# Performance work log

Measured on AMD Instinct MI355X. Metric: run time of the kernel, lower is better.

Reference implementation:

```python
import jax, jax.numpy as jnp
import numpy as np

C = 512          # in_channels == key_channels
K_REGIONS = 256  # number of proxy/object regions
N, H, Wd = 8, 128, 128


def _cba(x, w, sc, bi):
    """1x1 Conv + (folded) BN + ReLU. x: [n, Cin, h, w], w: [Cout, Cin]."""
    y = jnp.einsum('nchw,oc->nohw', x, w)
    return jax.nn.relu(sc[None, :, None, None] * y + bi[None, :, None, None])


def setup_inputs() -> dict:
    key = jax.random.key(0)
    kx, kp, kw, ks, kb = jax.random.split(key, 5)
    x = jax.random.normal(kx, (N, C, H, Wd), dtype=jnp.float32)
    proxy = jax.random.normal(kp, (N, C, K_REGIONS, 1), dtype=jnp.float32)
    # 7 ConvBnAct layers: [fp0, fp1, fo0, fo1, fd0, fd1, fup]
    W = jax.random.normal(kw, (7, C, C), dtype=jnp.float32) * (1.0 / np.sqrt(C))
    s = jax.random.uniform(ks, (7, C), dtype=jnp.float32, minval=0.5, maxval=1.5)
    b = jax.random.normal(kb, (7, C), dtype=jnp.float32) * 0.02
    return {'x': x, 'proxy': proxy, 'W': W, 's': s, 'b': b}


def reference(x, proxy, W, s, b):
    n, _, h, w = x.shape
    # f_pixel(x): two 1x1 ConvBnAct -> query [n, HW, C]
    q = _cba(_cba(x, W[0], s[0], b[0]), W[1], s[1], b[1])
    query = q.reshape(n, C, h * w).transpose(0, 2, 1)          # [n, HW, C]
    # f_object(proxy) -> key [n, C, K]
    k = _cba(_cba(proxy, W[2], s[2], b[2]), W[3], s[3], b[3])
    key_t = k.reshape(n, C, -1)                                 # [n, C, K]
    # f_down(proxy) -> value [n, K, C]
    v = _cba(_cba(proxy, W[4], s[4], b[4]), W[5], s[5], b[5])
    value = v.reshape(n, C, -1).transpose(0, 2, 1)              # [n, K, C]
    # scaled dot-product attention (single head, unmasked)
    sim = jnp.einsum('nqc,nck->nqk', query, key_t) * (C ** -0.5)
    sim = jax.nn.softmax(sim, axis=-1)                          # [n, HW, K]
    context = jnp.einsum('nqk,nkc->nqc', sim, value)            # [n, HW, C]
    context = context.transpose(0, 2, 1).reshape(n, C, h, w)
    # f_up
    return _cba(context, W[6], s[6], b[6])
```

## Files before the change

### kernel.cpp

```cpp
#include <hip/hip_runtime.h>
#include <hip/hip_bf16.h>
#include <stdint.h>

typedef __bf16 bf16;
typedef __bf16 bf16x8 __attribute__((ext_vector_type(8)));
typedef __bf16 bf16x4v __attribute__((ext_vector_type(4)));
typedef float f32x4 __attribute__((ext_vector_type(4)));

#define AS1 __attribute__((address_space(1)))
#define AS3 __attribute__((address_space(3)))

__device__ __forceinline__ void g2lds16(const bf16* g, bf16* l) {
  __builtin_amdgcn_global_load_lds((AS1 void*)(uintptr_t)g, (AS3 void*)l, 16, 0, 0);
}

__global__ void prep_weights_k(const float* __restrict__ W, const float* __restrict__ s,
                               const float* __restrict__ b, bf16* __restrict__ Wb,
                               float* __restrict__ bb) {
  int idx = blockIdx.x * 256 + threadIdx.x;
  int c = idx & 511;
  int o = (idx >> 9) & 511;
  int l = idx >> 18;
  const float r = 0.04419417382415922f;
  float f = (l == 3) ? r : 1.0f;
  Wb[idx] = (bf16)(W[idx] * s[(l << 9) + o] * f);
  if (c == 0) bb[(l << 9) + o] = b[(l << 9) + o] * f;
}

__global__ void transpose_cast_k(const float* __restrict__ in, bf16* __restrict__ out,
                                 int R, int Cc) {
  __shared__ float tile[32][33];
  int c0 = blockIdx.x * 32, r0 = blockIdx.y * 32;
  size_t zoff = (size_t)blockIdx.z * R * Cc;
  int tx = threadIdx.x, ty = threadIdx.y;
#pragma unroll
  for (int i = 0; i < 32; i += 8)
    tile[ty + i][tx] = in[zoff + (size_t)(r0 + ty + i) * Cc + c0 + tx];
  __syncthreads();
#pragma unroll
  for (int i = 0; i < 32; i += 8)
    out[zoff + (size_t)(c0 + ty + i) * R + r0 + tx] = (bf16)tile[tx][ty + i];
}

__global__ void softmax_k(const float* __restrict__ sim, bf16* __restrict__ P) {
  int row = blockIdx.x * 4 + (threadIdx.x >> 6);
  int lane = threadIdx.x & 63;
  const float4 v = ((const float4*)(sim + (size_t)row * 256))[lane];
  float m = fmaxf(fmaxf(v.x, v.y), fmaxf(v.z, v.w));
#pragma unroll
  for (int o = 32; o > 0; o >>= 1) m = fmaxf(m, __shfl_xor(m, o));
  float e0 = __expf(v.x - m), e1 = __expf(v.y - m);
  float e2 = __expf(v.z - m), e3 = __expf(v.w - m);
  float sum = e0 + e1 + e2 + e3;
#pragma unroll
  for (int o = 32; o > 0; o >>= 1) sum += __shfl_xor(sum, o);
  float inv = 1.0f / sum;
  bf16x4v pk;
  pk.x = (bf16)(e0 * inv); pk.y = (bf16)(e1 * inv);
  pk.z = (bf16)(e2 * inv); pk.w = (bf16)(e3 * inv);
  ((bf16x4v*)(P + (size_t)row * 256))[lane] = pk;
}

template <bool RELU, bool OUTF32, int BIASMODE>
__global__ __launch_bounds__(256, 2) void gemm_nt(
    const bf16* __restrict__ A, long sAb,
    const bf16* __restrict__ B, long sBb,
    void* __restrict__ OUT, long sOb,
    const float* __restrict__ bias,
    int M, int N, int Kd) {
  __shared__ bf16 sA[128][64];
  __shared__ bf16 sB[128][64];
  const int n0 = blockIdx.x * 128;
  const int m0 = blockIdx.y * 128;
  const bf16* Ab = A + (size_t)blockIdx.z * sAb;
  const bf16* Bb = B + (size_t)blockIdx.z * sBb;
  const int t = threadIdx.x;
  const int lane = t & 63;
  const int w = t >> 6;
  const int wm = (w & 1) << 6;
  const int wn = (w >> 1) << 6;
  const int srow = t >> 3;
  const int scol = (t & 7) << 3;

  f32x4 acc[4][4] = {};

  const int fr = lane & 15;
  const int fq = (lane >> 4) << 3;

  for (int k0 = 0; k0 < Kd; k0 += 64) {
#pragma unroll
    for (int i = 0; i < 4; i++) {
      g2lds16(Ab + (size_t)(m0 + i * 32 + srow) * Kd + (k0 + scol), &sA[i * 32 + srow][scol]);
      g2lds16(Bb + (size_t)(n0 + i * 32 + srow) * Kd + (k0 + scol), &sB[i * 32 + srow][scol]);
    }
    __syncthreads();
#pragma unroll
    for (int kk = 0; kk < 64; kk += 32) {
      bf16x8 af[4], bfv[4];
#pragma unroll
      for (int i = 0; i < 4; i++) af[i] = *(const bf16x8*)&sA[wm + i * 16 + fr][kk + fq];
#pragma unroll
      for (int j = 0; j < 4; j++) bfv[j] = *(const bf16x8*)&sB[wn + j * 16 + fr][kk + fq];
#pragma unroll
      for (int i = 0; i < 4; i++)
#pragma unroll
        for (int j = 0; j < 4; j++)
          acc[i][j] = __builtin_amdgcn_mfma_f32_16x16x32_bf16(af[i], bfv[j], acc[i][j], 0, 0, 0);
    }
    __syncthreads();
  }

  const int rb = m0 + wm + ((lane >> 4) << 2);
  const int cb = n0 + wn + (lane & 15);
#pragma unroll
  for (int i = 0; i < 4; i++) {
#pragma unroll
    for (int r = 0; r < 4; r++) {
      const int orow = rb + i * 16 + r;
#pragma unroll
      for (int j = 0; j < 4; j++) {
        const int oc = cb + j * 16;
        float vv = acc[i][j][r];
        if (BIASMODE == 1) vv += bias[oc];
        else if (BIASMODE == 2) vv += bias[orow];
        if (RELU) vv = fmaxf(vv, 0.0f);
        if (OUTF32)
          ((float*)OUT)[(size_t)blockIdx.z * sOb + (size_t)orow * N + oc] = vv;
        else
          ((bf16*)OUT)[(size_t)blockIdx.z * sOb + (size_t)orow * N + oc] = (bf16)vv;
      }
    }
  }
}

extern "C" void kernel_launch(void* const* d_in, const int* in_sizes, int n_in,
                              void* d_out, int out_size, void* d_ws, size_t ws_size,
                              hipStream_t stream) {
  const float* x = (const float*)d_in[0];
  const float* proxy = (const float*)d_in[1];
  const float* W = (const float*)d_in[2];
  const float* s = (const float*)d_in[3];
  const float* b = (const float*)d_in[4];
  float* out = (float*)d_out;

  const int C = 512, K = 256, NB = 8, HW = 16384;
  const size_t MiB = 1024 * 1024;
  char* ws = (char*)d_ws;
  if (ws_size < 272 * MiB) return;

  bf16* Wb   = (bf16*)(ws + 0);
  float* bb  = (float*)(ws + 3670016);
  bf16* pT   = (bf16*)(ws + 4 * MiB);
  bf16* k1   = (bf16*)(ws + 6 * MiB);
  bf16* key  = (bf16*)(ws + 8 * MiB);
  bf16* t2   = (bf16*)(ws + 10 * MiB);
  bf16* v    = (bf16*)(ws + 12 * MiB);
  bf16* bufA = (bf16*)(ws + 16 * MiB);
  bf16* bufB = (bf16*)(ws + 144 * MiB);

  bf16* xb  = bufA;
  bf16* t0  = bufB;
  bf16* q   = bufA;
  float* simf = (float*)bufB;
  bf16* P   = bufA;
  bf16* ctx = bufB;

  const long KC = (long)K * C;
  const long HWC = (long)HW * C;
  const long HWK = (long)HW * K;

  prep_weights_k<<<7 * 512 * 512 / 256, 256, 0, stream>>>(W, s, b, Wb, bb);
  transpose_cast_k<<<dim3(K / 32, C / 32, NB), dim3(32, 8), 0, stream>>>(proxy, pT, C, K);
  transpose_cast_k<<<dim3(HW / 32, C / 32, NB), dim3(32, 8), 0, stream>>>(x, xb, C, HW);
  gemm_nt<true, false, 1><<<dim3(C / 128, K / 128, NB), 256, 0, stream>>>(
      pT, KC, Wb + 2 * 262144, 0, k1, KC, bb + 2 * 512, K, C, C);
  gemm_nt<true, false, 1><<<dim3(C / 128, K / 128, NB), 256, 0, stream>>>(
      k1, KC, Wb + 3 * 262144, 0, key, KC, bb + 3 * 512, K, C, C);
  gemm_nt<true, false, 1><<<dim3(C / 128, K / 128, NB), 256, 0, stream>>>(
      pT, KC, Wb + 4 * 262144, 0, t2, KC, bb + 4 * 512, K, C, C);
  gemm_nt<true, false, 2><<<dim3(K / 128, C / 128, NB), 256, 0, stream>>>(
      Wb + 5 * 262144, 0, t2, KC, v, (long)C * K, bb + 5 * 512, C, K, C);
  gemm_nt<true, false, 1><<<dim3(C / 128, HW / 128, NB), 256, 0, stream>>>(
      xb, HWC, Wb, 0, t0, HWC, bb, HW, C, C);
  gemm_nt<true, false, 1><<<dim3(C / 128, HW / 128, NB), 256, 0, stream>>>(
      t0, HWC, Wb + 1 * 262144, 0, q, HWC, bb + 512, HW, C, C);
  gemm_nt<false, true, 0><<<dim3(K / 128, HW / 128, NB), 256, 0, stream>>>(
      q, HWC, key, KC, simf, HWK, nullptr, HW, K, C);
  softmax_k<<<NB * HW / 4, 256, 0, stream>>>(simf, P);
  gemm_nt<false, false, 0><<<dim3(C / 128, HW / 128, NB), 256, 0, stream>>>(
      P, HWK, v, (long)C * K, ctx, HWC, nullptr, HW, C, K);
  gemm_nt<true, true, 2><<<dim3(HW / 128, C / 128, NB), 256, 0, stream>>>(
      Wb + 6 * 262144, 0, ctx, HWC, out, HWC, bb + 6 * 512, C, HW, C);
}
```

Baseline: 1.017 ms.

## Fuse QK^T, softmax and PV into one attention kernel; merge proxy GEMMs

Replaces the separate sim GEMM (fp32 output), softmax kernel and PV GEMM with a single kernel. It computes a 64-row score tile in registers, applies softmax there and multiplies by V from LDS, so the large fp32 similarity matrix and the bf16 probability matrix never go through HBM. It also concatenates the fo0 and fd0 weights so both proxy first-layer convs run as one GEMM with strided leading dimensions. The transpose kernel is widened to 64x64 tiles with float4 loads. The risk is that the fused kernel rereads the full key and V per 64-row block with little overlap, and uses 64KB of LDS, which limits occupancy.

```diff
diff --git a/kernel.cpp b/kernel.cpp
--- a/kernel.cpp
+++ b/kernel.cpp
@@ -16,55 +16,54 @@
 
 __global__ void prep_weights_k(const float* __restrict__ W, const float* __restrict__ s,
                                const float* __restrict__ b, bf16* __restrict__ Wb,
-                               float* __restrict__ bb) {
+                               float* __restrict__ bb, bf16* __restrict__ W24,
+                               float* __restrict__ b24) {
   int idx = blockIdx.x * 256 + threadIdx.x;
   int c = idx & 511;
   int o = (idx >> 9) & 511;
   int l = idx >> 18;
   const float r = 0.04419417382415922f;
   float f = (l == 3) ? r : 1.0f;
-  Wb[idx] = (bf16)(W[idx] * s[(l << 9) + o] * f);
-  if (c == 0) bb[(l << 9) + o] = b[(l << 9) + o] * f;
+  float wv = W[idx] * s[(l << 9) + o] * f;
+  float bv = b[(l << 9) + o] * f;
+  Wb[idx] = (bf16)wv;
+  if (c == 0) bb[(l << 9) + o] = bv;
+  if (l == 2) { W24[(size_t)o * 512 + c] = (bf16)wv;         if (c == 0) b24[o] = bv; }
+  if (l == 4) { W24[(size_t)(512 + o) * 512 + c] = (bf16)wv; if (c == 0) b24[512 + o] = bv; }
 }
 
 __global__ void transpose_cast_k(const float* __restrict__ in, bf16* __restrict__ out,
-                                 int R, int Cc) {
-  __shared__ float tile[32][33];
-  int c0 = blockIdx.x * 32, r0 = blockIdx.y * 32;
-  size_t zoff = (size_t)blockIdx.z * R * Cc;
-  int tx = threadIdx.x, ty = threadIdx.y;
-#pragma unroll
-  for (int i = 0; i < 32; i += 8)
-    tile[ty + i][tx] = in[zoff + (size_t)(r0 + ty + i) * Cc + c0 + tx];
+                                 int R, int S) {
+  __shared__ float tile[64][65];
+  int s0 = blockIdx.x * 64, r0 = blockIdx.y * 64;
+  size_t zo = (size_t)blockIdx.z * R * S;
+  int t = threadIdx.x;
+  int rr = t >> 4, cc = t & 15;
+#pragma unroll
+  for (int i = 0; i < 4; i++) {
+    float4 v = *(const float4*)&in[zo + (size_t)(r0 + rr + 16 * i) * S + s0 + cc * 4];
+    tile[rr + 16 * i][cc * 4 + 0] = v.x;
+    tile[rr + 16 * i][cc * 4 + 1] = v.y;
+    tile[rr + 16 * i][cc * 4 + 2] = v.z;
+    tile[rr + 16 * i][cc * 4 + 3] = v.w;
+  }
   __syncthreads();
 #pragma unroll
-  for (int i = 0; i < 32; i += 8)
-    out[zoff + (size_t)(c0 + ty + i) * R + r0 + tx] = (bf16)tile[tx][ty + i];
-}
-
-__global__ void softmax_k(const float* __restrict__ sim, bf16* __restrict__ P) {
-  int row = blockIdx.x * 4 + (threadIdx.x >> 6);
-  int lane = threadIdx.x & 63;
-  const float4 v = ((const float4*)(sim + (size_t)row * 256))[lane];
-  float m = fmaxf(fmaxf(v.x, v.y), fmaxf(v.z, v.w));
-#pragma unroll
-  for (int o = 32; o > 0; o >>= 1) m = fmaxf(m, __shfl_xor(m, o));
-  float e0 = __expf(v.x - m), e1 = __expf(v.y - m);
-  float e2 = __expf(v.z - m), e3 = __expf(v.w - m);
-  float sum = e0 + e1 + e2 + e3;
-#pragma unroll
-  for (int o = 32; o > 0; o >>= 1) sum += __shfl_xor(sum, o);
-  float inv = 1.0f / sum;
-  bf16x4v pk;
-  pk.x = (bf16)(e0 * inv); pk.y = (bf16)(e1 * inv);
-  pk.z = (bf16)(e2 * inv); pk.w = (bf16)(e3 * inv);
-  ((bf16x4v*)(P + (size_t)row * 256))[lane] = pk;
+  for (int i = 0; i < 4; i++) {
+    int sR = rr + 16 * i;
+    bf16x4v o;
+    o.x = (bf16)tile[cc * 4 + 0][sR];
+    o.y = (bf16)tile[cc * 4 + 1][sR];
+    o.z = (bf16)tile[cc * 4 + 2][sR];
+    o.w = (bf16)tile[cc * 4 + 3][sR];
+    *(bf16x4v*)&out[zo + (size_t)(s0 + sR) * R + r0 + cc * 4] = o;
+  }
 }
 
 template <bool RELU, bool OUTF32, int BIASMODE>
 __global__ __launch_bounds__(256, 2) void gemm_nt(
-    const bf16* __restrict__ A, long sAb,
-    const bf16* __restrict__ B, long sBb,
+    const bf16* __restrict__ A, long sAb, int lda,
+    const bf16* __restrict__ B, long sBb, int ldb,
     void* __restrict__ OUT, long sOb,
     const float* __restrict__ bias,
     int M, int N, int Kd) {
@@ -83,15 +82,14 @@
   const int scol = (t & 7) << 3;
 
   f32x4 acc[4][4] = {};
-
   const int fr = lane & 15;
   const int fq = (lane >> 4) << 3;
 
   for (int k0 = 0; k0 < Kd; k0 += 64) {
 #pragma unroll
     for (int i = 0; i < 4; i++) {
-      g2lds16(Ab + (size_t)(m0 + i * 32 + srow) * Kd + (k0 + scol), &sA[i * 32 + srow][scol]);
-      g2lds16(Bb + (size_t)(n0 + i * 32 + srow) * Kd + (k0 + scol), &sB[i * 32 + srow][scol]);
+      g2lds16(Ab + (size_t)(m0 + i * 32 + srow) * lda + (k0 + scol), &sA[i * 32 + srow][scol]);
+      g2lds16(Bb + (size_t)(n0 + i * 32 + srow) * ldb + (k0 + scol), &sB[i * 32 + srow][scol]);
     }
     __syncthreads();
 #pragma unroll
@@ -133,6 +131,106 @@
   }
 }
 
+__global__ __launch_bounds__(256, 2) void flash_attn_k(
+    const bf16* __restrict__ Q, const bf16* __restrict__ Key,
+    const bf16* __restrict__ V, bf16* __restrict__ CTX) {
+  __shared__ char smraw[65536];
+  bf16 (*sq)[64]    = (bf16(*)[64])smraw;
+  bf16 (*skey)[64]  = (bf16(*)[64])(smraw + 8192);
+  bf16 (*sP)[256]   = (bf16(*)[256])smraw;
+  bf16 (*sv)[256]   = (bf16(*)[256])(smraw + 32768);
+
+  const int t = threadIdx.x;
+  const int lane = t & 63;
+  const int w = t >> 6;
+  const int m0 = blockIdx.x * 64;
+  const size_t zq = (size_t)blockIdx.y * 16384 * 512;
+  const size_t zk = (size_t)blockIdx.y * 256 * 512;
+  const bf16* Qz = Q + zq;
+  const bf16* Kz = Key + zk;
+  const bf16* Vz = V + zk;
+  bf16* Cz = CTX + zq;
+
+  const int fr = lane & 15;
+  const int quad = lane >> 4;
+  const int fq = quad << 3;
+
+  f32x4 accS[16] = {};
+  {
+    const int srow = t >> 3;
+    const int scol = (t & 7) << 3;
+    for (int k0 = 0; k0 < 512; k0 += 64) {
+#pragma unroll
+      for (int i = 0; i < 2; i++)
+        g2lds16(Qz + (size_t)(m0 + i * 32 + srow) * 512 + k0 + scol, &sq[i * 32 + srow][scol]);
+#pragma unroll
+      for (int i = 0; i < 8; i++)
+        g2lds16(Kz + (size_t)(i * 32 + srow) * 512 + k0 + scol, &skey[i * 32 + srow][scol]);
+      __syncthreads();
+#pragma unroll
+      for (int kk = 0; kk < 64; kk += 32) {
+        bf16x8 aq = *(const bf16x8*)&sq[w * 16 + fr][kk + fq];
+#pragma unroll
+        for (int j = 0; j < 16; j++) {
+          bf16x8 bk = *(const bf16x8*)&skey[j * 16 + fr][kk + fq];
+          accS[j] = __builtin_amdgcn_mfma_f32_16x16x32_bf16(aq, bk, accS[j], 0, 0, 0);
+        }
+      }
+      __syncthreads();
+    }
+  }
+
+#pragma unroll
+  for (int r = 0; r < 4; r++) {
+    float m = accS[0][r];
+#pragma unroll
+    for (int j = 1; j < 16; j++) m = fmaxf(m, accS[j][r]);
+#pragma unroll
+    for (int o = 1; o < 16; o <<= 1) m = fmaxf(m, __shfl_xor(m, o));
+    float sum = 0.0f;
+#pragma unroll
+    for (int j = 0; j < 16; j++) { float e = __expf(accS[j][r] - m); accS[j][r] = e; sum += e; }
+#pragma unroll
+    for (int o = 1; o < 16; o <<= 1) sum += __shfl_xor(sum, o);
+    float inv = 1.0f / sum;
+#pragma unroll
+    for (int j = 0; j < 16; j++) accS[j][r] *= inv;
+  }
+
+#pragma unroll
+  for (int j = 0; j < 16; j++)
+#pragma unroll
+    for (int r = 0; r < 4; r++)
+      sP[w * 16 + quad * 4 + r][j * 16 + fr] = (bf16)accS[j][r];
+
+  {
+    const int srow = t >> 5;
+    const int scol = (t & 31) << 3;
+    for (int c0 = 0; c0 < 512; c0 += 64) {
+#pragma unroll
+      for (int i = 0; i < 8; i++)
+        g2lds16(Vz + (size_t)(c0 + i * 8 + srow) * 256 + scol, &sv[i * 8 + srow][scol]);
+      __syncthreads();
+      f32x4 accC[4] = {};
+#pragma unroll
+      for (int kk = 0; kk < 256; kk += 32) {
+        bf16x8 ap = *(const bf16x8*)&sP[w * 16 + fr][kk + fq];
+#pragma unroll
+        for (int j = 0; j < 4; j++) {
+          bf16x8 bv = *(const bf16x8*)&sv[j * 16 + fr][kk + fq];
+          accC[j] = __builtin_amdgcn_mfma_f32_16x16x32_bf16(ap, bv, accC[j], 0, 0, 0);
+        }
+      }
+#pragma unroll
+      for (int j = 0; j < 4; j++)
+#pragma unroll
+        for (int r = 0; r < 4; r++)
+          Cz[(size_t)(m0 + w * 16 + quad * 4 + r) * 512 + c0 + j * 16 + fr] = (bf16)accC[j][r];
+      __syncthreads();
+    }
+  }
+}
+
 extern "C" void kernel_launch(void* const* d_in, const int* in_sizes, int n_in,
                               void* d_out, int out_size, void* d_ws, size_t ws_size,
                               hipStream_t stream) {
@@ -150,45 +248,38 @@
 
   bf16* Wb   = (bf16*)(ws + 0);
   float* bb  = (float*)(ws + 3670016);
-  bf16* pT   = (bf16*)(ws + 4 * MiB);
-  bf16* k1   = (bf16*)(ws + 6 * MiB);
-  bf16* key  = (bf16*)(ws + 8 * MiB);
-  bf16* t2   = (bf16*)(ws + 10 * MiB);
-  bf16* v    = (bf16*)(ws + 12 * MiB);
+  bf16* W24  = (bf16*)(ws + 4 * MiB);
+  float* b24 = (float*)(ws + 5 * MiB);
+  bf16* pT   = (bf16*)(ws + 6 * MiB);
+  bf16* kt   = (bf16*)(ws + 8 * MiB);
+  bf16* key  = (bf16*)(ws + 12 * MiB);
+  bf16* v    = (bf16*)(ws + 14 * MiB);
   bf16* bufA = (bf16*)(ws + 16 * MiB);
   bf16* bufB = (bf16*)(ws + 144 * MiB);
 
   bf16* xb  = bufA;
   bf16* t0  = bufB;
   bf16* q   = bufA;
-  float* simf = (float*)bufB;
-  bf16* P   = bufA;
   bf16* ctx = bufB;
 
   const long KC = (long)K * C;
+  const long KT = (long)K * 1024;
   const long HWC = (long)HW * C;
-  const long HWK = (long)HW * K;
-
-  prep_weights_k<<<7 * 512 * 512 / 256, 256, 0, stream>>>(W, s, b, Wb, bb);
-  transpose_cast_k<<<dim3(K / 32, C / 32, NB), dim3(32, 8), 0, stream>>>(proxy, pT, C, K);
-  transpose_cast_k<<<dim3(HW / 32, C / 32, NB), dim3(32, 8), 0, stream>>>(x, xb, C, HW);
+
+  prep_weights_k<<<7 * 512 * 512 / 256, 256, 0, stream>>>(W, s, b, Wb, bb, W24, b24);
+  transpose_cast_k<<<dim3(K / 64, C / 64, NB), 256, 0, stream>>>(proxy, pT, C, K);
+  transpose_cast_k<<<dim3(HW / 64, C / 64, NB), 256, 0, stream>>>(x, xb, C, HW);
+  gemm_nt<true, false, 1><<<dim3(1024 / 128, K / 128, NB), 256, 0, stream>>>(
+      pT, KC, C, W24, 0, C, kt, KT, b24, K, 1024, C);
   gemm_nt<true, false, 1><<<dim3(C / 128, K / 128, NB), 256, 0, stream>>>(
-      pT, KC, Wb + 2 * 262144, 0, k1, KC, bb + 2 * 512, K, C, C);
-  gemm_nt<true, false, 1><<<dim3(C / 128, K / 128, NB), 256, 0, stream>>>(
-      k1, KC, Wb + 3 * 262144, 0, key, KC, bb + 3 * 512, K, C, C);
-  gemm_nt<true, false, 1><<<dim3(C / 128, K / 128, NB), 256, 0, stream>>>(
-      pT, KC, Wb + 4 * 262144, 0, t2, KC, bb + 4 * 512, K, C, C);
+      kt, KT, 1024, Wb + 3 * 262144, 0, C, key, KC, bb + 3 * 512, K, C, C);
   gemm_nt<true, false, 2><<<dim3(K / 128, C / 128, NB), 256, 0, stream>>>(
-      Wb + 5 * 262144, 0, t2, KC, v, (long)C * K, bb + 5 * 512, C, K, C);
+      Wb + 5 * 262144, 0, C, kt + 512, KT, 1024, v, KC, bb + 5 * 512, C, K, C);
   gemm_nt<true, false, 1><<<dim3(C / 128, HW / 128, NB), 256, 0, stream>>>(
-      xb, HWC, Wb, 0, t0, HWC, bb, HW, C, C);
+      xb, HWC, C, Wb, 0, C, t0, HWC, bb, HW, C, C);
   gemm_nt<true, false, 1><<<dim3(C / 128, HW / 128, NB), 256, 0, stream>>>(
-      t0, HWC, Wb + 1 * 262144, 0, q, HWC, bb + 512, HW, C, C);
-  gemm_nt<false, true, 0><<<dim3(K / 128, HW / 128, NB), 256, 0, stream>>>(
-      q, HWC, key, KC, simf, HWK, nullptr, HW, K, C);
-  softmax_k<<<NB * HW / 4, 256, 0, stream>>>(simf, P);
-  gemm_nt<false, false, 0><<<dim3(C / 128, HW / 128, NB), 256, 0, stream>>>(
-      P, HWK, v, (long)C * K, ctx, HWC, nullptr, HW, C, K);
+      t0, HWC, C, Wb + 1 * 262144, 0, C, q, HWC, bb + 512, HW, C, C);
+  flash_attn_k<<<dim3(HW / 64, NB), 256, 0, stream>>>(q, key, v, ctx);
   gemm_nt<true, true, 2><<<dim3(HW / 128, C / 128, NB), 256, 0, stream>>>(
-      Wb + 6 * 262144, 0, ctx, HWC, out, HWC, bb + 6 * 512, C, HW, C);
-}
+      Wb + 6 * 262144, 0, C, ctx, HWC, C, out, HWC, bb + 6 * 512, C, HW, C);
+}
```

After: 1.080 ms. 6.2% more time.
